# Kernel optimization log

Hardware: AMD Instinct MI355X
Metric: run time of the kernel (lower is better)

## Reference

```python
import jax, jax.numpy as jnp
import numpy as np

B, H, N = 256, 128, 2048

def setup_inputs() -> dict:
    key = jax.random.key(0)
    k1, k2, k3, k4, k5 = jax.random.split(key, 5)
    return {
        "static_hidden": jax.random.normal(k1, (B, H, N), dtype=jnp.float32),
        "dynamic_hidden": jax.random.normal(k2, (B, H, N), dtype=jnp.float32),
        "decoder_hidden": jax.random.normal(k3, (B, H), dtype=jnp.float32),
        "v": jax.random.normal(k4, (1, 1, H), dtype=jnp.float32) * 0.05,
        "W": jax.random.normal(k5, (1, H, 3 * H), dtype=jnp.float32) * 0.05,
    }

def reference(static_hidden, dynamic_hidden, decoder_hidden, v, W):
    # hidden: [B, 3H, N] = concat(static, dynamic, broadcast(decoder))
    dec = jnp.broadcast_to(decoder_hidden[:, :, None], static_hidden.shape)
    hidden = jnp.concatenate((static_hidden, dynamic_hidden, dec), axis=1)
    # W @ hidden: [B, H, N]; tanh; v @ .: [B, 1, N]
    Wh = jnp.tanh(jnp.einsum('hk,bkn->bhn', W[0], hidden))
    scores = jnp.einsum('h,bhn->bn', v[0, 0], Wh)[:, None, :]  # [B,1,N]
    return jax.nn.softmax(scores, axis=2)
```

## Files before the change

### kernel.cpp

```cpp
#include <hip/hip_runtime.h>
#include <cstddef>

#define Bn 256
#define Hd 128
#define Nd 2048
#define K3 384
#define K2 256

typedef _Float16 half8 __attribute__((ext_vector_type(8)));
typedef float    float4v __attribute__((ext_vector_type(4)));

__device__ __forceinline__ float fast_tanh(float x) {
    return 1.0f - __fdividef(2.0f, __expf(2.0f * x) + 1.0f);
}

__global__ void prep_w16(const float* __restrict__ W, _Float16* __restrict__ Wf) {
    int idx = blockIdx.x * 256 + threadIdx.x;
    int h = idx >> 8, k = idx & 255;
    Wf[idx] = (_Float16)W[h * K3 + k];
}

__global__ void prep_c(const float* __restrict__ W, const float* __restrict__ dec,
                       float* __restrict__ cb) {
    __shared__ float dl[Hd];
    int b = blockIdx.x;
    int h = threadIdx.x;
    dl[h] = dec[b * Hd + h];
    __syncthreads();
    float acc = 0.f;
    #pragma unroll 8
    for (int k = 0; k < Hd; ++k)
        acc = fmaf(W[h * K3 + 256 + k], dl[k], acc);
    cb[b * Hd + h] = acc;
}

__global__ __launch_bounds__(256, 2)
void score_kernel(const float* __restrict__ shp, const float* __restrict__ dhp,
                  const _Float16* __restrict__ Wf, const float* __restrict__ cbp,
                  const float* __restrict__ v, float* __restrict__ out) {
    __shared__ __align__(16) _Float16 xl[128 * 256];
    __shared__ float red[4 * 128];

    const int tid  = threadIdx.x;
    const int w    = __builtin_amdgcn_readfirstlane(tid >> 6);
    const int lane = tid & 63;
    const int qd   = lane >> 4;
    const int ln   = lane & 15;
    const int b    = blockIdx.y;
    const int n0   = blockIdx.x * 128;
    const int h0   = w * 32;

    half8 Af[2][8];
    #pragma unroll
    for (int Mt = 0; Mt < 2; ++Mt) {
        const _Float16* wp = Wf + ((h0 + Mt * 16 + ln) << 8) + qd * 8;
        #pragma unroll
        for (int kt = 0; kt < 8; ++kt)
            Af[Mt][kt] = *reinterpret_cast<const half8*>(wp + kt * 32);
    }

    float4v acc[2][8];
    #pragma unroll
    for (int Mt = 0; Mt < 2; ++Mt) {
        float4v c4 = *reinterpret_cast<const float4v*>(cbp + b * Hd + h0 + Mt * 16 + qd * 4);
        #pragma unroll
        for (int Nt = 0; Nt < 8; ++Nt) acc[Mt][Nt] = c4;
    }

    {
        const int n1  = 2 * lane;
        const int swz = lane & 7;
        #pragma unroll
        for (int hf = 0; hf < 2; ++hf) {
            const float* src = (hf ? dhp : shp) + (size_t)b * (Hd * (size_t)Nd) + n0 + n1;
            #pragma unroll
            for (int i = 0; i < 4; ++i) {
                const int kl = i * 32 + w * 8;
                float2 xv[8];
                #pragma unroll
                for (int j = 0; j < 8; ++j)
                    xv[j] = *reinterpret_cast<const float2*>(src + (size_t)(kl + j) * Nd);
                half8 e0, e1;
                #pragma unroll
                for (int j = 0; j < 8; ++j) {
                    e0[j] = (_Float16)xv[j].x;
                    e1[j] = (_Float16)xv[j].y;
                }
                const int ck = (hf * 128 + kl) >> 3;
                const int p  = ck ^ swz;
                *reinterpret_cast<half8*>(&xl[n1 * 256 + p * 8])       = e0;
                *reinterpret_cast<half8*>(&xl[(n1 + 1) * 256 + p * 8]) = e1;
            }
        }
    }
    __syncthreads();

    const int swr = (ln >> 1) & 7;
    #pragma unroll
    for (int kt = 0; kt < 8; ++kt) {
        half8 Bf[8];
        const int ckb = kt * 4 + qd;
        #pragma unroll
        for (int Nt = 0; Nt < 8; ++Nt) {
            const int row = Nt * 16 + ln;
            Bf[Nt] = *reinterpret_cast<const half8*>(&xl[row * 256 + ((ckb ^ swr) << 3)]);
        }
        #pragma unroll
        for (int Nt = 0; Nt < 8; ++Nt) {
            acc[0][Nt] = __builtin_amdgcn_mfma_f32_16x16x32_f16(Af[0][kt], Bf[Nt], acc[0][Nt], 0, 0, 0);
            acc[1][Nt] = __builtin_amdgcn_mfma_f32_16x16x32_f16(Af[1][kt], Bf[Nt], acc[1][Nt], 0, 0, 0);
        }
    }

    float4v v0 = *reinterpret_cast<const float4v*>(v + h0 + qd * 4);
    float4v v1 = *reinterpret_cast<const float4v*>(v + h0 + 16 + qd * 4);
    #pragma unroll
    for (int Nt = 0; Nt < 8; ++Nt) {
        float part = 0.f;
        #pragma unroll
        for (int r = 0; r < 4; ++r) {
            part = fmaf(v0[r], fast_tanh(acc[0][Nt][r]), part);
            part = fmaf(v1[r], fast_tanh(acc[1][Nt][r]), part);
        }
        part += __shfl_xor(part, 16);
        part += __shfl_xor(part, 32);
        if (qd == 0) red[w * 128 + Nt * 16 + ln] = part;
    }
    __syncthreads();
    if (tid < 128) {
        float s = red[tid] + red[128 + tid] + red[256 + tid] + red[384 + tid];
        out[(size_t)b * Nd + n0 + tid] = s;
    }
}

__global__ void softmax_k(float* __restrict__ out) {
    int b = blockIdx.x;
    float* row = out + (size_t)b * Nd;
    int tid = threadIdx.x;

    float loc[8];
    float mx = -3.4e38f;
    #pragma unroll
    for (int i = 0; i < 8; ++i) {
        loc[i] = row[tid + (i << 8)];
        mx = fmaxf(mx, loc[i]);
    }
    #pragma unroll
    for (int off = 32; off > 0; off >>= 1) mx = fmaxf(mx, __shfl_xor(mx, off));
    __shared__ float s4[4];
    if ((tid & 63) == 0) s4[tid >> 6] = mx;
    __syncthreads();
    mx = fmaxf(fmaxf(s4[0], s4[1]), fmaxf(s4[2], s4[3]));

    float sum = 0.f;
    #pragma unroll
    for (int i = 0; i < 8; ++i) {
        loc[i] = __expf(loc[i] - mx);
        sum += loc[i];
    }
    #pragma unroll
    for (int off = 32; off > 0; off >>= 1) sum += __shfl_xor(sum, off);
    __shared__ float s4b[4];
    if ((tid & 63) == 0) s4b[tid >> 6] = sum;
    __syncthreads();
    sum = s4b[0] + s4b[1] + s4b[2] + s4b[3];

    float inv = 1.0f / sum;
    #pragma unroll
    for (int i = 0; i < 8; ++i) row[tid + (i << 8)] = loc[i] * inv;
}

extern "C" void kernel_launch(void* const* d_in, const int* in_sizes, int n_in,
                              void* d_out, int out_size, void* d_ws, size_t ws_size,
                              hipStream_t stream) {
    const float* shp = (const float*)d_in[0];
    const float* dhp = (const float*)d_in[1];
    const float* dec = (const float*)d_in[2];
    const float* v   = (const float*)d_in[3];
    const float* W   = (const float*)d_in[4];
    float* out = (float*)d_out;

    _Float16* Wf = (_Float16*)d_ws;
    float* cbp = (float*)((char*)d_ws + 65536);

    hipLaunchKernelGGL(prep_w16, dim3(128), dim3(256), 0, stream, W, Wf);
    hipLaunchKernelGGL(prep_c,   dim3(Bn),  dim3(Hd),  0, stream, W, dec, cbp);
    hipLaunchKernelGGL(score_kernel, dim3(Nd / 128, Bn), dim3(256), 0, stream,
                       shp, dhp, Wf, cbp, v, out);
    hipLaunchKernelGGL(softmax_k, dim3(Bn), dim3(256), 0, stream, out);
}
```

Before: 519.3 us.

## Split K into two halves to halve LDS tile and raise occupancy

The score kernel now stages the static and dynamic halves of K through a half-size LDS buffer (32KB instead of 64KB), one after the other, with a barrier between them. W fragments are loaded per half, so fewer registers are live, and launch bounds go up to 3 blocks per CU. Global loads change from float2 to float4 per lane with a new XOR swizzle. Each block now does an extra sync and a serialized load-then-compute phase in exchange for more resident blocks to hide memory latency.

```diff
diff --git a/kernel.cpp b/kernel.cpp
--- a/kernel.cpp
+++ b/kernel.cpp
@@ -5,7 +5,6 @@
 #define Hd 128
 #define Nd 2048
 #define K3 384
-#define K2 256
 
 typedef _Float16 half8 __attribute__((ext_vector_type(8)));
 typedef float    float4v __attribute__((ext_vector_type(4)));
@@ -34,11 +33,11 @@
     cb[b * Hd + h] = acc;
 }
 
-__global__ __launch_bounds__(256, 2)
+__global__ __launch_bounds__(256, 3)
 void score_kernel(const float* __restrict__ shp, const float* __restrict__ dhp,
                   const _Float16* __restrict__ Wf, const float* __restrict__ cbp,
                   const float* __restrict__ v, float* __restrict__ out) {
-    __shared__ __align__(16) _Float16 xl[128 * 256];
+    __shared__ __align__(16) _Float16 xl[128 * 128];
     __shared__ float red[4 * 128];
 
     const int tid  = threadIdx.x;
@@ -50,14 +49,8 @@
     const int n0   = blockIdx.x * 128;
     const int h0   = w * 32;
 
-    half8 Af[2][8];
-    #pragma unroll
-    for (int Mt = 0; Mt < 2; ++Mt) {
-        const _Float16* wp = Wf + ((h0 + Mt * 16 + ln) << 8) + qd * 8;
-        #pragma unroll
-        for (int kt = 0; kt < 8; ++kt)
-            Af[Mt][kt] = *reinterpret_cast<const half8*>(wp + kt * 32);
-    }
+    const int nn = lane & 31;
+    const int kk = lane >> 5;
 
     float4v acc[2][8];
     #pragma unroll
@@ -67,48 +60,53 @@
         for (int Nt = 0; Nt < 8; ++Nt) acc[Mt][Nt] = c4;
     }
 
-    {
-        const int n1  = 2 * lane;
-        const int swz = lane & 7;
+    for (int half = 0; half < 2; ++half) {
+        const float* src = (half ? dhp : shp) + (size_t)b * (Hd * (size_t)Nd) + n0;
+        if (half) __syncthreads();
+
         #pragma unroll
-        for (int hf = 0; hf < 2; ++hf) {
-            const float* src = (hf ? dhp : shp) + (size_t)b * (Hd * (size_t)Nd) + n0 + n1;
+        for (int g = 0; g < 2; ++g) {
+            const int kl = w * 32 + g * 16 + kk * 8;
+            float4v xv[8];
             #pragma unroll
-            for (int i = 0; i < 4; ++i) {
-                const int kl = i * 32 + w * 8;
-                float2 xv[8];
+            for (int j = 0; j < 8; ++j)
+                xv[j] = *reinterpret_cast<const float4v*>(src + (size_t)(kl + j) * Nd + 4 * nn);
+            const int ck = kl >> 3;
+            #pragma unroll
+            for (int r = 0; r < 4; ++r) {
+                half8 e;
                 #pragma unroll
-                for (int j = 0; j < 8; ++j)
-                    xv[j] = *reinterpret_cast<const float2*>(src + (size_t)(kl + j) * Nd);
-                half8 e0, e1;
-                #pragma unroll
-                for (int j = 0; j < 8; ++j) {
-                    e0[j] = (_Float16)xv[j].x;
-                    e1[j] = (_Float16)xv[j].y;
-                }
-                const int ck = (hf * 128 + kl) >> 3;
-                const int p  = ck ^ swz;
-                *reinterpret_cast<half8*>(&xl[n1 * 256 + p * 8])       = e0;
-                *reinterpret_cast<half8*>(&xl[(n1 + 1) * 256 + p * 8]) = e1;
+                for (int j = 0; j < 8; ++j) e[j] = (_Float16)xv[j][r];
+                const int row  = 4 * nn + r;
+                const int phys = ck ^ (row & 15) ^ (row >> 4);
+                *reinterpret_cast<half8*>(&xl[row * 128 + phys * 8]) = e;
             }
         }
-    }
-    __syncthreads();
 
-    const int swr = (ln >> 1) & 7;
-    #pragma unroll
-    for (int kt = 0; kt < 8; ++kt) {
-        half8 Bf[8];
-        const int ckb = kt * 4 + qd;
+        half8 Af[2][4];
         #pragma unroll
-        for (int Nt = 0; Nt < 8; ++Nt) {
-            const int row = Nt * 16 + ln;
-            Bf[Nt] = *reinterpret_cast<const half8*>(&xl[row * 256 + ((ckb ^ swr) << 3)]);
+        for (int Mt = 0; Mt < 2; ++Mt) {
+            const _Float16* wp = Wf + ((h0 + Mt * 16 + ln) << 8) + half * 128 + qd * 8;
+            #pragma unroll
+            for (int kt = 0; kt < 4; ++kt)
+                Af[Mt][kt] = *reinterpret_cast<const half8*>(wp + kt * 32);
         }
+        __syncthreads();
+
         #pragma unroll
-        for (int Nt = 0; Nt < 8; ++Nt) {
-            acc[0][Nt] = __builtin_amdgcn_mfma_f32_16x16x32_f16(Af[0][kt], Bf[Nt], acc[0][Nt], 0, 0, 0);
-            acc[1][Nt] = __builtin_amdgcn_mfma_f32_16x16x32_f16(Af[1][kt], Bf[Nt], acc[1][Nt], 0, 0, 0);
+        for (int kt = 0; kt < 4; ++kt) {
+            half8 Bf[8];
+            #pragma unroll
+            for (int Nt = 0; Nt < 8; ++Nt) {
+                const int row  = Nt * 16 + ln;
+                const int phys = (kt * 4 + qd) ^ ln ^ Nt;
+                Bf[Nt] = *reinterpret_cast<const half8*>(&xl[row * 128 + phys * 8]);
+            }
+            #pragma unroll
+            for (int Nt = 0; Nt < 8; ++Nt) {
+                acc[0][Nt] = __builtin_amdgcn_mfma_f32_16x16x32_f16(Af[0][kt], Bf[Nt], acc[0][Nt], 0, 0, 0);
+                acc[1][Nt] = __builtin_amdgcn_mfma_f32_16x16x32_f16(Af[1][kt], Bf[Nt], acc[1][Nt], 0, 0, 0);
+            }
         }
     }
 
```

New measurement: 546.7 us. 5.3% more time.
